# Kernel optimization log

Hardware: AMD Instinct MI355X
Metric: run time of the kernel (lower is better)

The kernel has to match this reference:

```python
import jax, jax.numpy as jnp
import numpy as np

# Model dims (match init_kwargs)
HID = 1024   # hidden_size
H   = 16     # num_heads
DK  = 64     # head_dim (key)
DV  = 128    # head value dim = int(head_dim * expand_v)
VAL = H * DV # value_dim = 2048
CONV = 4     # short conv kernel size
EPS = 1e-6
NORM_EPS = 1e-5


def _causal_conv_silu(x, w):
    # x: [B,T,C], w: [C,K] depthwise causal conv, no bias, silu activation
    T = x.shape[1]
    K = w.shape[1]
    xp = jnp.pad(x, ((0, 0), (K - 1, 0), (0, 0)))
    y = sum(xp[:, i:i + T, :] * w[:, i] for i in range(K))
    return jax.nn.silu(y)


def setup_inputs() -> dict:
    key = jax.random.key(0)
    ks = jax.random.split(key, 16)
    s = 0.02
    rn = lambda k, sh: jax.random.normal(k, sh, jnp.float32)
    return {
        'hidden_states': rn(ks[0], (1, 2048, HID)),
        'norm_w': jnp.ones((HID,), jnp.float32),
        'q_w': rn(ks[1], (H * DK, HID)) * s,
        'k_w': rn(ks[2], (H * DK, HID)) * s,
        'v_w': rn(ks[3], (VAL, HID)) * s,
        'a_w': rn(ks[4], (H, HID)) * s,
        'b_w': rn(ks[5], (H, HID)) * s,
        'g_w': rn(ks[6], (VAL, HID)) * s,
        'dt_bias': jax.random.uniform(ks[7], (H,), jnp.float32, -2.0, 0.0),
        'A_log': jnp.log(jax.random.uniform(ks[8], (H,), jnp.float32, 1.0, 8.0)),
        'conv_q_w': rn(ks[9], (H * DK, CONV)) * 0.2,
        'conv_k_w': rn(ks[10], (H * DK, CONV)) * 0.2,
        'conv_v_w': rn(ks[11], (VAL, CONV)) * 0.2,
        'o_norm_w': jnp.ones((DV,), jnp.float32),
        'o_proj_w': rn(ks[12], (HID, VAL)) * s,
        'out_proj_w': rn(ks[13], (HID, HID)) * s,
    }


def reference(hidden_states, norm_w, q_w, k_w, v_w, a_w, b_w, g_w, dt_bias,
              A_log, conv_q_w, conv_k_w, conv_v_w, o_norm_w, o_proj_w, out_proj_w):
    B, T, D = hidden_states.shape
    # RMSNorm
    x = hidden_states * jax.lax.rsqrt(
        jnp.mean(hidden_states * hidden_states, -1, keepdims=True) + EPS) * norm_w

    # projections + causal depthwise short conv + silu
    q = _causal_conv_silu(x @ q_w.T, conv_q_w).reshape(B, T, H, DK)
    k = _causal_conv_silu(x @ k_w.T, conv_k_w).reshape(B, T, H, DK)
    v = _causal_conv_silu(x @ v_w.T, conv_v_w).reshape(B, T, H, DV)

    beta = jax.nn.sigmoid(x @ b_w.T)                       # [B,T,H]
    g = -jnp.exp(A_log) * jax.nn.softplus(x @ a_w.T + dt_bias)  # [B,T,H] log-decay

    # rank-1 DC removal on keys: (I - 1 1^T / DK) k, i.e. subtract per-head mean
    k = k - jnp.mean(k, -1, keepdims=True)

    # L2 normalize q, k along head dim; scale q
    q = q * jax.lax.rsqrt(jnp.sum(q * q, -1, keepdims=True) + EPS)
    k = k * jax.lax.rsqrt(jnp.sum(k * k, -1, keepdims=True) + EPS)
    q = q * (DK ** -0.5)

    # gated delta-rule recurrence over time (time-major scan)
    qT = q.transpose(1, 0, 2, 3)
    kT = k.transpose(1, 0, 2, 3)
    vT = v.transpose(1, 0, 2, 3)
    bT = beta.transpose(1, 0, 2)
    gT = g.transpose(1, 0, 2)

    def step(S, inp):
        qt, kt, vt, bt, gt = inp              # S: [B,H,DK,DV]
        S = S * jnp.exp(gt)[..., None, None]
        v_new = (vt - jnp.einsum('bhk,bhkv->bhv', kt, S)) * bt[..., None]
        S = S + jnp.einsum('bhk,bhv->bhkv', kt, v_new)
        o = jnp.einsum('bhk,bhkv->bhv', qt, S)
        return S, o

    S0 = jnp.zeros((B, H, DK, DV), x.dtype)
    _, oT = jax.lax.scan(step, S0, (qT, kT, vT, bT, gT))
    o = oT.transpose(1, 0, 2, 3)                           # [B,T,H,DV]

    # gated RMSNorm on output heads
    gate = (x @ g_w.T).reshape(B, T, H, DV)
    o = o * jax.lax.rsqrt(jnp.mean(o * o, -1, keepdims=True) + NORM_EPS) * o_norm_w
    o = o * jax.nn.silu(gate)

    o = o.reshape(B, T, VAL) @ o_proj_w.T                  # [B,T,HID]
    return o @ out_proj_w.T
```

## Files before the change

kernel.cpp:

```cpp
#include <hip/hip_runtime.h>
#include <math.h>

#define S72 72

typedef __bf16 bf16;
typedef __bf16 bf16x8 __attribute__((ext_vector_type(8)));
typedef __bf16 bf16x4v __attribute__((ext_vector_type(4)));
typedef __bf16 bf16x2v __attribute__((ext_vector_type(2)));
typedef float f32x4 __attribute__((ext_vector_type(4)));

__device__ __forceinline__ float wredsum(float v) {
#pragma unroll
  for (int off = 32; off > 0; off >>= 1) v += __shfl_xor(v, off, 64);
  return v;
}
__device__ __forceinline__ float sigmoidf_(float x) { return 1.f / (1.f + __expf(-x)); }

__device__ __forceinline__ int sxy(int row, int col) {
  return (row << 6) + ((((col >> 3) ^ (row & 7)) << 3) | (col & 7));
}
__device__ __forceinline__ int sx8(int row, int chunk) {
  return (row << 6) + ((chunk ^ (row & 7)) << 3);
}

__global__ __launch_bounds__(256) void k_pre(const float* __restrict__ h,
    const float* __restrict__ nw, const float* __restrict__ aw,
    const float* __restrict__ bw, const float* __restrict__ dtb,
    const float* __restrict__ alog, bf16* __restrict__ xb,
    float* __restrict__ graw, float* __restrict__ btb,
    const float* __restrict__ qw, const float* __restrict__ kw,
    const float* __restrict__ vw, const float* __restrict__ gw,
    const float* __restrict__ opw, const float* __restrict__ ow,
    bf16* qwb, bf16* kwb, bf16* vwb, bf16* gwb, bf16* opwb, bf16* owb) {
  __shared__ float red[4];
  __shared__ __align__(16) float xs[1024];
  int tid = threadIdx.x;
  if (blockIdx.x >= 2048) {
    long cb = blockIdx.x - 2048;
    for (long u = cb*256 + tid; u < 2359296; u += 4608l*256) {
      const float* src; bf16* dst; long l;
      if      (u <  262144) { src=qw;  dst=qwb;  l=u; }
      else if (u <  524288) { src=kw;  dst=kwb;  l=u-262144; }
      else if (u < 1048576) { src=vw;  dst=vwb;  l=u-524288; }
      else if (u < 1572864) { src=gw;  dst=gwb;  l=u-1048576; }
      else if (u < 2097152) { src=opw; dst=opwb; l=u-1572864; }
      else                  { src=ow;  dst=owb;  l=u-2097152; }
      float4 s = *(const float4*)(src + l*4);
      bf16x4v b; b[0]=(bf16)s.x; b[1]=(bf16)s.y; b[2]=(bf16)s.z; b[3]=(bf16)s.w;
      *(bf16x4v*)(dst + l*4) = b;
    }
    return;
  }
  int t = blockIdx.x;
  float4 hv = *(const float4*)(h + (size_t)t*1024 + tid*4);
  float ss = hv.x*hv.x + hv.y*hv.y + hv.z*hv.z + hv.w*hv.w;
  float wsum = wredsum(ss);
  if ((tid & 63) == 0) red[tid >> 6] = wsum;
  __syncthreads();
  float tot = red[0] + red[1] + red[2] + red[3];
  float rs = rsqrtf(tot * (1.f/1024.f) + 1e-6f);
  float4 w4 = *(const float4*)(nw + tid*4);
  float4 y;
  y.x = hv.x*rs*w4.x; y.y = hv.y*rs*w4.y; y.z = hv.z*rs*w4.z; y.w = hv.w*rs*w4.w;
  *(float4*)(xs + tid*4) = y;
  bf16x4v b; b[0]=(bf16)y.x; b[1]=(bf16)y.y; b[2]=(bf16)y.z; b[3]=(bf16)y.w;
  *(bf16x4v*)(xb + (size_t)t*1024 + tid*4) = b;
  __syncthreads();
  int wave = tid >> 6, lane = tid & 63;
  const float4* x4 = (const float4*)xs;
#pragma unroll
  for (int hi = 0; hi < 4; ++hi) {
    int hh = wave*4 + hi;
    float sa = 0.f, sb = 0.f;
#pragma unroll
    for (int i = 0; i < 4; ++i) {
      float4 xv = x4[i*64 + lane];
      float4 av = *(const float4*)(aw + hh*1024 + i*256 + lane*4);
      float4 bv = *(const float4*)(bw + hh*1024 + i*256 + lane*4);
      sa += xv.x*av.x + xv.y*av.y + xv.z*av.z + xv.w*av.w;
      sb += xv.x*bv.x + xv.y*bv.y + xv.z*bv.z + xv.w*bv.w;
    }
    sa = wredsum(sa); sb = wredsum(sb);
    if (lane == 0) {
      float ap = sa + dtb[hh];
      float sp = (ap > 20.f) ? ap : log1pf(expf(ap));
      graw[t*16 + hh] = -expf(alog[hh]) * sp;
      btb[t*16 + hh] = 1.f / (1.f + expf(-sb));
    }
  }
}

template <typename OutT>
__device__ __forceinline__ void gemm_body(const bf16* __restrict__ A,
    const bf16* __restrict__ B, OutT* __restrict__ C, int N, int K, int m0, int n0) {
  __shared__ bf16 As[2][128*32];
  __shared__ bf16 Bs[2][128*32];
  const int tid = threadIdx.x, lane = tid & 63, wave = tid >> 6;
  const int wm = (wave >> 1) * 64, wn = (wave & 1) * 64;
  const int srow = wave*16 + (lane >> 2);
  const int swl = (((lane & 3) ^ ((lane >> 3) & 3))) * 8;
  const int sdst = (lane & 3) * 8;
  const int quad = lane >> 4, l16 = lane & 15;
  const int sw = (l16 >> 1) & 3;
  f32x4 acc[4][4] = {};
  const int nk = K >> 5;
#pragma unroll
  for (int i = 0; i < 2; ++i) {
    int r = i*64 + srow;
    __builtin_amdgcn_global_load_lds(
      (__attribute__((address_space(1))) void*)(A + (size_t)(m0 + r)*K + swl),
      (__attribute__((address_space(3))) void*)(&As[0][r*32 + sdst]), 16, 0, 0);
    __builtin_amdgcn_global_load_lds(
      (__attribute__((address_space(1))) void*)(B + (size_t)(n0 + r)*K + swl),
      (__attribute__((address_space(3))) void*)(&Bs[0][r*32 + sdst]), 16, 0, 0);
  }
  for (int kt = 0; kt < nk; ++kt) {
    const int cur = kt & 1;
    __syncthreads();
    bf16x8 af[4], bfr[4];
#pragma unroll
    for (int mt = 0; mt < 4; ++mt)
      af[mt] = *(const bf16x8*)(&As[cur][(wm + mt*16 + l16)*32 + (quad ^ sw)*8]);
#pragma unroll
    for (int nt = 0; nt < 4; ++nt)
      bfr[nt] = *(const bf16x8*)(&Bs[cur][(wn + nt*16 + l16)*32 + (quad ^ sw)*8]);
    if (kt + 1 < nk) {
      int k0 = (kt + 1) << 5;
#pragma unroll
      for (int i = 0; i < 2; ++i) {
        int r = i*64 + srow;
        __builtin_amdgcn_global_load_lds(
          (__attribute__((address_space(1))) void*)(A + (size_t)(m0 + r)*K + k0 + swl),
          (__attribute__((address_space(3))) void*)(&As[cur^1][r*32 + sdst]), 16, 0, 0);
        __builtin_amdgcn_global_load_lds(
          (__attribute__((address_space(1))) void*)(B + (size_t)(n0 + r)*K + k0 + swl),
          (__attribute__((address_space(3))) void*)(&Bs[cur^1][r*32 + sdst]), 16, 0, 0);
      }
    }
#pragma unroll
    for (int mt = 0; mt < 4; ++mt)
#pragma unroll
      for (int nt = 0; nt < 4; ++nt)
        acc[mt][nt] = __builtin_amdgcn_mfma_f32_16x16x32_bf16(af[mt], bfr[nt], acc[mt][nt], 0, 0, 0);
  }
#pragma unroll
  for (int mt = 0; mt < 4; ++mt)
#pragma unroll
    for (int nt = 0; nt < 4; ++nt)
#pragma unroll
      for (int r = 0; r < 4; ++r) {
        int row = m0 + wm + mt*16 + quad*4 + r;
        int col = n0 + wn + nt*16 + l16;
        C[(size_t)row*N + col] = (OutT)acc[mt][nt][r];
      }
}

__global__ __launch_bounds__(256) void k_gemm_proj(const bf16* __restrict__ A,
    const bf16* __restrict__ qwb, const bf16* __restrict__ kwb,
    const bf16* __restrict__ vwb, const bf16* __restrict__ gwb,
    bf16* __restrict__ qpre, bf16* __restrict__ kpre,
    bf16* __restrict__ vpre, bf16* __restrict__ gpre) {
  int bx = blockIdx.x;
  const bf16* B; bf16* C; int N, xt;
  if      (bx <  8) { B = qwb; C = qpre; N = 1024; xt = bx; }
  else if (bx < 16) { B = kwb; C = kpre; N = 1024; xt = bx - 8; }
  else if (bx < 32) { B = vwb; C = vpre; N = 2048; xt = bx - 16; }
  else              { B = gwb; C = gpre; N = 2048; xt = bx - 32; }
  gemm_body<bf16>(A, B, C, N, 1024, blockIdx.y*128, xt*128);
}

template <typename OutT>
__global__ __launch_bounds__(256) void k_gemm_bt64(const bf16* __restrict__ A,
    const bf16* __restrict__ B, OutT* __restrict__ C, int N, int K) {
  __shared__ bf16 As[2][128*32];
  __shared__ bf16 Bs[2][64*32];
  const int tid = threadIdx.x, lane = tid & 63, wave = tid >> 6;
  const int wm = wave * 32;
  const int srow = wave*16 + (lane >> 2);
  const int swl = (((lane & 3) ^ ((lane >> 3) & 3))) * 8;
  const int sdst = (lane & 3) * 8;
  const int quad = lane >> 4, l16 = lane & 15;
  const int sw = (l16 >> 1) & 3;
  const int m0 = blockIdx.y * 128, n0 = blockIdx.x * 64;
  f32x4 acc[2][4] = {};
  const int nk = K >> 5;
#pragma unroll
  for (int i = 0; i < 2; ++i) {
    int r = i*64 + srow;
    __builtin_amdgcn_global_load_lds(
      (__attribute__((address_space(1))) void*)(A + (size_t)(m0 + r)*K + swl),
      (__attribute__((address_space(3))) void*)(&As[0][r*32 + sdst]), 16, 0, 0);
  }
  __builtin_amdgcn_global_load_lds(
    (__attribute__((address_space(1))) void*)(B + (size_t)(n0 + srow)*K + swl),
    (__attribute__((address_space(3))) void*)(&Bs[0][srow*32 + sdst]), 16, 0, 0);
  for (int kt = 0; kt < nk; ++kt) {
    const int cur = kt & 1;
    __syncthreads();
    bf16x8 af[2], bfr[4];
#pragma unroll
    for (int mt = 0; mt < 2; ++mt)
      af[mt] = *(const bf16x8*)(&As[cur][(wm + mt*16 + l16)*32 + (quad ^ sw)*8]);
#pragma unroll
    for (int nt = 0; nt < 4; ++nt)
      bfr[nt] = *(const bf16x8*)(&Bs[cur][(nt*16 + l16)*32 + (quad ^ sw)*8]);
    if (kt + 1 < nk) {
      int k0 = (kt + 1) << 5;
#pragma unroll
      for (int i = 0; i < 2; ++i) {
        int r = i*64 + srow;
        __builtin_amdgcn_global_load_lds(
          (__attribute__((address_space(1))) void*)(A + (size_t)(m0 + r)*K + k0 + swl),
          (__attribute__((address_space(3))) void*)(&As[cur^1][r*32 + sdst]), 16, 0, 0);
      }
      __builtin_amdgcn_global_load_lds(
        (__attribute__((address_space(1))) void*)(B + (size_t)(n0 + srow)*K + k0 + swl),
        (__attribute__((address_space(3))) void*)(&Bs[cur^1][srow*32 + sdst]), 16, 0, 0);
    }
#pragma unroll
    for (int mt = 0; mt < 2; ++mt)
#pragma unroll
      for (int nt = 0; nt < 4; ++nt)
        acc[mt][nt] = __builtin_amdgcn_mfma_f32_16x16x32_bf16(af[mt], bfr[nt], acc[mt][nt], 0, 0, 0);
  }
#pragma unroll
  for (int mt = 0; mt < 2; ++mt)
#pragma unroll
    for (int nt = 0; nt < 4; ++nt)
#pragma unroll
      for (int r = 0; r < 4; ++r) {
        int row = m0 + wm + mt*16 + quad*4 + r;
        int col = n0 + nt*16 + l16;
        C[(size_t)row*N + col] = (OutT)acc[mt][nt][r];
      }
}

template<int NT>
__device__ __forceinline__ void mm_band(const bf16* A_lds, const bf16* B_lds,
    int w16, int cb, int l16, int quad, f32x4* acc) {
#pragma unroll
  for (int n = 0; n < NT; ++n) { acc[n][0]=0.f; acc[n][1]=0.f; acc[n][2]=0.f; acc[n][3]=0.f; }
#pragma unroll
  for (int kt = 0; kt < 2; ++kt) {
    bf16x8 af = *(const bf16x8*)(A_lds + sx8(w16 + l16, kt*4 + quad));
#pragma unroll
    for (int n = 0; n < NT; ++n) {
      bf16x8 bf = *(const bf16x8*)(B_lds + sx8(cb + n*16 + l16, kt*4 + quad));
      acc[n] = __builtin_amdgcn_mfma_f32_16x16x32_bf16(af, bf, acc[n], 0, 0, 0);
    }
  }
}

__global__ __launch_bounds__(512) void k_prepass(
    const bf16* __restrict__ qpre, const bf16* __restrict__ kpre,
    const bf16* __restrict__ vpre, const float* __restrict__ cqw,
    const float* __restrict__ ckw, const float* __restrict__ cvw,
    const float* __restrict__ graw, const float* __restrict__ beta,
    bf16* __restrict__ EF, float* __restrict__ dSl, float* __restrict__ obuf) {
  const int bx = blockIdx.x, c = bx >> 4, h = bx & 15, tid = threadIdx.x;
  const int t0 = c * 64;
  const int wave = tid >> 6, lane = tid & 63, l16 = lane & 15, quad = lane >> 4;
  const int w16 = (wave >> 1) * 16;
  const int chh = wave & 1;
  const int r0 = wave * 8;

  __shared__ bf16 SM[36864];
  __shared__ float bs[64], bts_s[64], es[64], gms[64];
  bf16* Kr    = SM;
  bf16* powR0 = SM + 4096;
  bf16* prod0 = SM + 8192;
  bf16* T2T   = SM + 12288;
  bf16* powT0 = SM + 16384;
  bf16* powR1 = SM + 20480;
  bf16* powT1 = SM + 24576;
  bf16* prod1 = SM + 28672;
  bf16* qbf   = SM + 32768;
  bf16* VT   = SM;
  bf16* VlT  = SM + 8192;
  bf16* KT   = powT0;
  bf16* KbT  = powR1;
  bf16* Pm   = powT1;
  bf16* WR   = prod0;
  bf16* Mrow = prod1;

  if (tid < 64) {
    float g = graw[(size_t)(t0 + tid)*16 + h];
    float b = g;
#pragma unroll
    for (int off = 1; off < 64; off <<= 1) {
      float p = __shfl_up(b, off, 64);
      if (tid >= off) b += p;
    }
    bs[tid] = b;
    bts_s[tid] = beta[(size_t)(t0 + tid)*16 + h];
    float b63 = __shfl(b, 63, 64);
    es[tid] = __expf(b63 - b);
    gms[tid] = __expf(b);
  }

  float kreg[8], vreg[16];
  {
    float4 wq  = *(const float4*)(cqw + (h*64 + lane)*4);
    float4 wk  = *(const float4*)(ckw + (h*64 + lane)*4);
    float tv[11];
#pragma unroll
    for (int j = 0; j < 11; ++j) {
      int tg = t0 + r0 + j - 3;
      tv[j] = (tg >= 0) ? (float)qpre[(size_t)tg*1024 + h*64 + lane] : 0.f;
    }
#pragma unroll
    for (int rr = 0; rr < 8; ++rr) {
      float y = tv[rr]*wq.x + tv[rr+1]*wq.y + tv[rr+2]*wq.z + tv[rr+3]*wq.w;
      y = y * sigmoidf_(y);
      float ssq = wredsum(y*y);
      y *= rsqrtf(ssq + 1e-6f) * 0.125f;
      qbf[sxy(r0+rr, lane)] = (bf16)y;
    }
#pragma unroll
    for (int j = 0; j < 11; ++j) {
      int tg = t0 + r0 + j - 3;
      tv[j] = (tg >= 0) ? (float)kpre[(size_t)tg*1024 + h*64 + lane] : 0.f;
    }
#pragma unroll
    for (int rr = 0; rr < 8; ++rr) {
      float y = tv[rr]*wk.x + tv[rr+1]*wk.y + tv[rr+2]*wk.z + tv[rr+3]*wk.w;
      y = y * sigmoidf_(y);
      float m = wredsum(y) * (1.f/64.f);
      y -= m;
      float ssq = wredsum(y*y);
      y *= rsqrtf(ssq + 1e-6f);
      kreg[rr] = y;
      Kr[sxy(r0+rr, lane)] = (bf16)y;
    }
#pragma unroll
    for (int hf = 0; hf < 2; ++hf) {
      float4 wv = *(const float4*)(cvw + (h*128 + hf*64 + lane)*4);
#pragma unroll
      for (int j = 0; j < 11; ++j) {
        int tg = t0 + r0 + j - 3;
        tv[j] = (tg >= 0) ? (float)vpre[(size_t)tg*2048 + h*128 + hf*64 + lane] : 0.f;
      }
#pragma unroll
      for (int rr = 0; rr < 8; ++rr) {
        float y = tv[rr]*wv.x + tv[rr+1]*wv.y + tv[rr+2]*wv.z + tv[rr+3]*wv.w;
        vreg[hf*8+rr] = y * sigmoidf_(y);
      }
    }
  }
  __syncthreads();

  {
    f32x4 acc[2];
    mm_band<2>(Kr, Kr, w16, chh*32, l16, quad, acc);
#pragma unroll
    for (int n = 0; n < 2; ++n) {
      int col = chh*32 + n*16 + l16;
      bf16x4v tv;
#pragma unroll
      for (int r = 0; r < 4; ++r) {
        int row = w16 + quad*4 + r;
        float nv = 0.f;
        if (row > col) nv = -bts_s[row] * __expf(bs[row] - bs[col]) * acc[n][r];
        bf16 nb = (bf16)nv;
        powR0[sxy(row, col)] = nb;
        tv[r] = nb;
        prod0[sxy(row, col)] = (row == col) ? (bf16)1.f : nb;
      }
      *(bf16x4v*)(powT0 + sxy(col, w16 + quad*4)) = tv;
    }
  }
  __syncthreads();

  int pc = 0, rc = 0;
#pragma unroll 1
  for (int i = 1; i <= 5; ++i) {
    bf16* sqA = pc ? powR1 : powR0;
    bf16* sqB = pc ? powT1 : powT0;
    bf16* sqRo = pc ? powR0 : powR1;
    bf16* sqTo = pc ? powT0 : powT1;
    {
      f32x4 acc[2];
      mm_band<2>(sqA, sqB, w16, chh*32, l16, quad, acc);
#pragma unroll
      for (int n = 0; n < 2; ++n) {
        int col = chh*32 + n*16 + l16;
        bf16x4v tv;
#pragma unroll
        for (int r = 0; r < 4; ++r) {
          int row = w16 + quad*4 + r;
          bf16 vb = (bf16)acc[n][r];
          sqRo[sxy(row, col)] = vb;
          tv[r] = vb;
        }
        *(bf16x4v*)(sqTo + sxy(col, w16 + quad*4)) = tv;
      }
    }
    __syncthreads();
    bf16* prA = rc ? prod1 : prod0;
    bf16* prO = rc ? prod0 : prod1;
    {
      f32x4 acc[2];
      mm_band<2>(prA, sqTo, w16, chh*32, l16, quad, acc);
#pragma unroll
      for (int n = 0; n < 2; ++n) {
        int col = chh*32 + n*16 + l16;
        bf16x4v tv;
#pragma unroll
        for (int r = 0; r < 4; ++r) {
          int row = w16 + quad*4 + r;
          float val = acc[n][r] + (float)prA[sxy(row, col)];
          prO[sxy(row, col)] = (bf16)val;
          tv[r] = (bf16)(val * bts_s[col] * gms[col]);
        }
        if (i == 5) *(bf16x4v*)(T2T + sxy(col, w16 + quad*4)) = tv;
      }
    }
    __syncthreads();
    pc ^= 1; rc ^= 1;
  }

#pragma unroll
  for (int rr = 0; rr < 8; ++rr) {
    KT[sxy(lane, r0+rr)]  = (bf16)kreg[rr];
    KbT[sxy(lane, r0+rr)] = (bf16)(kreg[rr] * es[r0+rr]);
  }
  {
    f32x4 acc[2];
#pragma unroll
    for (int n = 0; n < 2; ++n) { acc[n][0]=0.f; acc[n][1]=0.f; acc[n][2]=0.f; acc[n][3]=0.f; }
#pragma unroll
    for (int kt = 0; kt < 2; ++kt) {
      bf16x8 af = *(const bf16x8*)(qbf + sx8(w16 + l16, kt*4 + quad));
#pragma unroll
      for (int n = 0; n < 2; ++n) {
        bf16x8 bf = *(const bf16x8*)(Kr + sx8(chh*32 + n*16 + l16, kt*4 + quad));
        acc[n] = __builtin_amdgcn_mfma_f32_16x16x32_bf16(af, bf, acc[n], 0, 0, 0);
      }
    }
#pragma unroll
    for (int n = 0; n < 2; ++n) {
      int col = chh*32 + n*16 + l16;
#pragma unroll
      for (int r = 0; r < 4; ++r) {
        int row = w16 + quad*4 + r;
        float pv = (row >= col) ? __expf(bs[row] - bs[col]) * acc[n][r] : 0.f;
        Pm[sxy(row, col)] = (bf16)pv;
      }
    }
  }
  __syncthreads();

  {
    f32x4 acc[2];
    mm_band<2>(KbT, T2T, w16, chh*32, l16, quad, acc);
#pragma unroll
    for (int n = 0; n < 2; ++n) {
      int col = chh*32 + n*16 + l16;
#pragma unroll
      for (int r = 0; r < 4; ++r)
        WR[sxy(w16 + quad*4 + r, col)] = (bf16)acc[n][r];
    }
  }
#pragma unroll
  for (int hf = 0; hf < 2; ++hf)
#pragma unroll
    for (int rr = 0; rr < 8; ++rr)
      VT[sxy(hf*64 + lane, r0+rr)] = (bf16)(bts_s[r0+rr] * vreg[hf*8+rr]);
  __syncthreads();
  {
    f32x4 acc[2];
    mm_band<2>(WR, KT, w16, chh*32, l16, quad, acc);
    float gC = gms[63];
    size_t eb = (size_t)bx * 13824;
#pragma unroll
    for (int n = 0; n < 2; ++n) {
      int col = chh*32 + n*16 + l16;
#pragma unroll
      for (int r = 0; r < 4; ++r) {
        int row = w16 + quad*4 + r;
        float ev = ((row == col) ? gC : 0.f) - acc[n][r];
        bf16 eh = (bf16)ev;
        EF[eb + row*S72 + col] = eh;
        EF[eb + 4608 + row*S72 + col] = (bf16)(ev - (float)eh);
      }
    }
  }
  __syncthreads();
  {
    f32x4 acc[2];
    mm_band<2>(Pm, T2T, w16, chh*32, l16, quad, acc);
#pragma unroll
    for (int n = 0; n < 2; ++n) {
      int col = chh*32 + n*16 + l16;
#pragma unroll
      for (int r = 0; r < 4; ++r)
        WR[sxy(w16 + quad*4 + r, col)] = (bf16)acc[n][r];
    }
  }
  __syncthreads();
  {
    f32x4 acc[2];
    mm_band<2>(WR, KT, w16, chh*32, l16, quad, acc);
    size_t eb = (size_t)bx * 13824;
#pragma unroll
    for (int n = 0; n < 2; ++n) {
      int col = chh*32 + n*16 + l16;
#pragma unroll
      for (int r = 0; r < 4; ++r) {
        int row = w16 + quad*4 + r;
        float qv = (float)qbf[sxy(row, col)];
        EF[eb + 9216 + row*S72 + col] = (bf16)(gms[row]*qv - acc[n][r]);
      }
    }
  }
  __syncthreads();
  {
    f32x4 acc[4];
    mm_band<4>(Mrow, VT, w16, chh*64, l16, quad, acc);
#pragma unroll
    for (int n = 0; n < 4; ++n) {
      int col = chh*64 + n*16 + l16;
      bf16x4v tv;
#pragma unroll
      for (int r = 0; r < 4; ++r) tv[r] = (bf16)acc[n][r];
      *(bf16x4v*)(VlT + sxy(col, w16 + quad*4)) = tv;
    }
  }
  __syncthreads();
  {
    f32x4 acc[4];
    mm_band<4>(KbT, VlT, w16, chh*64, l16, quad, acc);
#pragma unroll
    for (int n = 0; n < 4; ++n) {
      int col = chh*64 + n*16 + l16;
#pragma unroll
      for (int r = 0; r < 4; ++r)
        dSl[(size_t)bx*8192 + (size_t)(w16 + quad*4 + r)*128 + col] = acc[n][r];
    }
  }
  {
    f32x4 acc[4];
    mm_band<4>(Pm, VlT, w16, chh*64, l16, quad, acc);
#pragma unroll
    for (int n = 0; n < 4; ++n) {
      int col = chh*64 + n*16 + l16;
#pragma unroll
      for (int r = 0; r < 4; ++r)
        obuf[(size_t)(t0 + w16 + quad*4 + r)*2048 + h*128 + col] = acc[n][r];
    }
  }
}

__global__ __launch_bounds__(256) void k_seq(const bf16* __restrict__ EF,
    const float* __restrict__ dSl, float* __restrict__ osb) {
  const int bid = blockIdx.x;
  const int h = (bid & 7) + 8*((bid >> 3) & 1);
  const int dq = bid >> 4;
  const int tid = threadIdx.x, wave = tid >> 6, lane = tid & 63;
  const int l16 = lane & 15, quad = lane >> 4;
  const int mb = wave * 16;
  __shared__ bf16 Sthi[32*S72], Stlo[32*S72];
  for (int i = tid; i < 2304; i += 256) { Sthi[i] = (bf16)0.f; Stlo[i] = (bf16)0.f; }

  const size_t arow = (size_t)(mb + l16)*S72 + quad*8;
  const size_t drow = (size_t)dq*32 + (size_t)(mb + quad*4)*128 + l16;

  bf16x8 eh[2][2], el[2][2], ff[2][2];
  float dsv[2][8];

  auto loadEF = [&](int c, int sl) {
    const bf16* base = EF + (size_t)(c*16 + h)*13824 + arow;
#pragma unroll
    for (int kt = 0; kt < 2; ++kt) {
      eh[sl][kt] = *(const bf16x8*)(base + kt*32);
      el[sl][kt] = *(const bf16x8*)(base + 4608 + kt*32);
      ff[sl][kt] = *(const bf16x8*)(base + 9216 + kt*32);
    }
    const float* db = dSl + (size_t)(c*16 + h)*8192 + drow;
#pragma unroll
    for (int nt = 0; nt < 2; ++nt)
#pragma unroll
      for (int r = 0; r < 4; ++r)
        dsv[sl][nt*4+r] = db[(size_t)r*128 + nt*16];
  };

  loadEF(0, 0);
  asm volatile("s_waitcnt lgkmcnt(0)" ::: "memory");
  __builtin_amdgcn_s_barrier();

#pragma unroll 2
  for (int c = 0; c < 32; ++c) {
    const int cur = c & 1, nxt = cur ^ 1;
    bf16x8 bh[2][2], bl[2][2];
#pragma unroll
    for (int nt = 0; nt < 2; ++nt)
#pragma unroll
      for (int kt = 0; kt < 2; ++kt) {
        bh[nt][kt] = *(const bf16x8*)(Sthi + (nt*16 + l16)*S72 + kt*32 + quad*8);
        bl[nt][kt] = *(const bf16x8*)(Stlo + (nt*16 + l16)*S72 + kt*32 + quad*8);
      }
    if (c + 1 < 32) loadEF(c + 1, nxt);

    f32x4 accS[2], accO[2];
#pragma unroll
    for (int nt = 0; nt < 2; ++nt) {
#pragma unroll
      for (int r = 0; r < 4; ++r) accS[nt][r] = dsv[cur][nt*4+r];
      accO[nt][0]=0.f; accO[nt][1]=0.f; accO[nt][2]=0.f; accO[nt][3]=0.f;
    }
#pragma unroll
    for (int kt = 0; kt < 2; ++kt) {
#pragma unroll
      for (int nt = 0; nt < 2; ++nt) {
        accS[nt] = __builtin_amdgcn_mfma_f32_16x16x32_bf16(eh[cur][kt], bh[nt][kt], accS[nt], 0, 0, 0);
        accS[nt] = __builtin_amdgcn_mfma_f32_16x16x32_bf16(eh[cur][kt], bl[nt][kt], accS[nt], 0, 0, 0);
        accS[nt] = __builtin_amdgcn_mfma_f32_16x16x32_bf16(el[cur][kt], bh[nt][kt], accS[nt], 0, 0, 0);
        accO[nt] = __builtin_amdgcn_mfma_f32_16x16x32_bf16(ff[cur][kt], bh[nt][kt], accO[nt], 0, 0, 0);
        accO[nt] = __builtin_amdgcn_mfma_f32_16x16x32_bf16(ff[cur][kt], bl[nt][kt], accO[nt], 0, 0, 0);
      }
    }
    asm volatile("s_waitcnt lgkmcnt(0)" ::: "memory");
    __builtin_amdgcn_s_barrier();
    {
      int t0 = c*64;
#pragma unroll
      for (int nt = 0; nt < 2; ++nt)
#pragma unroll
        for (int r = 0; r < 4; ++r)
          osb[(size_t)(t0 + mb + quad*4 + r)*2048 + h*128 + dq*32 + nt*16 + l16] = accO[nt][r];
    }
#pragma unroll
    for (int nt = 0; nt < 2; ++nt) {
      bf16x4v hv, lv;
#pragma unroll
      for (int r = 0; r < 4; ++r) {
        float v = accS[nt][r];
        bf16 hb = (bf16)v;
        hv[r] = hb;
        lv[r] = (bf16)(v - (float)hb);
      }
      *(bf16x4v*)(Sthi + (nt*16 + l16)*S72 + mb + quad*4) = hv;
      *(bf16x4v*)(Stlo + (nt*16 + l16)*S72 + mb + quad*4) = lv;
    }
    asm volatile("s_waitcnt lgkmcnt(0)" ::: "memory");
    __builtin_amdgcn_s_barrier();
  }
}

__global__ __launch_bounds__(64) void k_gatenorm(const float* __restrict__ o,
    const float* __restrict__ os, const bf16* __restrict__ gpre,
    const float* __restrict__ onw, bf16* __restrict__ og) {
  int t = blockIdx.x, hh = blockIdx.y, lane = threadIdx.x;
  size_t base = (size_t)t*2048 + hh*128 + lane*2;
  float2 o2 = *(const float2*)(o + base);
  float2 s2 = *(const float2*)(os + base);
  o2.x += s2.x; o2.y += s2.y;
  float ss = wredsum(o2.x*o2.x + o2.y*o2.y);
  float rs = rsqrtf(ss * (1.f/128.f) + 1e-5f);
  float2 nw = *(const float2*)(onw + lane*2);
  bf16x2v g2 = *(const bf16x2v*)(gpre + base);
  float g0 = (float)g2[0], g1 = (float)g2[1];
  float r0 = o2.x * rs * nw.x * (g0 * sigmoidf_(g0));
  float r1 = o2.y * rs * nw.y * (g1 * sigmoidf_(g1));
  bf16x2v b; b[0] = (bf16)r0; b[1] = (bf16)r1;
  *(bf16x2v*)(og + base) = b;
}

extern "C" void kernel_launch(void* const* d_in, const int* in_sizes, int n_in,
                              void* d_out, int out_size, void* d_ws, size_t ws_size,
                              hipStream_t stream) {
  const float* hs   = (const float*)d_in[0];
  const float* nw   = (const float*)d_in[1];
  const float* qw   = (const float*)d_in[2];
  const float* kw   = (const float*)d_in[3];
  const float* vw   = (const float*)d_in[4];
  const float* aw   = (const float*)d_in[5];
  const float* bw   = (const float*)d_in[6];
  const float* gw   = (const float*)d_in[7];
  const float* dtb  = (const float*)d_in[8];
  const float* alog = (const float*)d_in[9];
  const float* cqw  = (const float*)d_in[10];
  const float* ckw  = (const float*)d_in[11];
  const float* cvw  = (const float*)d_in[12];
  const float* onw  = (const float*)d_in[13];
  const float* opw  = (const float*)d_in[14];
  const float* ow   = (const float*)d_in[15];
  float* out = (float*)d_out;

  char* p = (char*)d_ws;
  auto alloc = [&](size_t bytes) { char* r = p; p += (bytes + 255) & ~255ull; return r; };
  bf16*  xb    = (bf16*) alloc((size_t)2048*1024*2);
  bf16*  qwb   = (bf16*) alloc((size_t)1024*1024*2);
  bf16*  kwb   = (bf16*) alloc((size_t)1024*1024*2);
  bf16*  vwb   = (bf16*) alloc((size_t)2048*1024*2);
  bf16*  gwb   = (bf16*) alloc((size_t)2048*1024*2);
  bf16*  opwb  = (bf16*) alloc((size_t)1024*2048*2);
  bf16*  owb   = (bf16*) alloc((size_t)1024*1024*2);
  bf16*  qpre  = (bf16*) alloc((size_t)2048*1024*2);
  bf16*  kpre  = (bf16*) alloc((size_t)2048*1024*2);
  bf16*  vpre  = (bf16*) alloc((size_t)2048*2048*2);
  bf16*  gpre  = (bf16*) alloc((size_t)2048*2048*2);
  float* graw  = (float*)alloc((size_t)2048*16*4);
  float* btb   = (float*)alloc((size_t)2048*16*4);
  float* ob    = (float*)alloc((size_t)2048*2048*4);
  bf16*  ogb   = (bf16*) alloc((size_t)2048*2048*2);
  bf16*  h1b   = (bf16*) alloc((size_t)2048*1024*2);
  bf16*  EF    = (bf16*) alloc((size_t)512*13824*2);
  float* osb   = (float*)alloc((size_t)512*8192*4);
  float* dSl   = (float*)xb;

  k_pre<<<2048+4608, 256, 0, stream>>>(hs, nw, aw, bw, dtb, alog, xb, graw, btb,
                                       qw, kw, vw, gw, opw, ow,
                                       qwb, kwb, vwb, gwb, opwb, owb);
  k_gemm_proj<<<dim3(48,16,1), 256, 0, stream>>>(xb, qwb, kwb, vwb, gwb, qpre, kpre, vpre, gpre);
  k_prepass<<<512, 512, 0, stream>>>(qpre, kpre, vpre, cqw, ckw, cvw, graw, btb, EF, dSl, ob);
  k_seq<<<64, 256, 0, stream>>>(EF, dSl, osb);
  k_gatenorm<<<dim3(2048,16,1), 64, 0, stream>>>(ob, osb, gpre, onw, ogb);
  k_gemm_bt64<bf16><<<dim3(16,16,1), 256, 0, stream>>>(ogb, opwb, h1b, 1024, 2048);
  k_gemm_bt64<float><<<dim3(16,16,1), 256, 0, stream>>>(h1b, owb, out, 1024, 1024);
}
```

Before: 272.0 us.

## Double-buffer state in sequential scan, split MFMA chains, batch conv loads in prepass

The sequential chunk kernel now keeps the bf16 hi/lo state in two LDS buffers, ping-ponging between them. This removes one of the two barriers per chunk, and the five MFMA products use independent accumulators so the dependent MFMA chains are shorter. In the prepass, the q/k/v conv input loads are issued together up front, and the k mean and variance reductions run in one fused shuffle loop; launch bounds now carry an occupancy hint. The changes add LDS use and register pressure, and the one-pass variance formula is slightly less numerically robust.

```diff
diff --git a/kernel.cpp b/kernel.cpp
--- a/kernel.cpp
+++ b/kernel.cpp
@@ -251,7 +251,7 @@
   }
 }
 
-__global__ __launch_bounds__(512) void k_prepass(
+__global__ __launch_bounds__(512, 4) void k_prepass(
     const bf16* __restrict__ qpre, const bf16* __restrict__ kpre,
     const bf16* __restrict__ vpre, const float* __restrict__ cqw,
     const float* __restrict__ ckw, const float* __restrict__ cvw,
@@ -302,49 +302,49 @@
   {
     float4 wq  = *(const float4*)(cqw + (h*64 + lane)*4);
     float4 wk  = *(const float4*)(ckw + (h*64 + lane)*4);
-    float tv[11];
+    float4 wv0 = *(const float4*)(cvw + (h*128 + lane)*4);
+    float4 wv1 = *(const float4*)(cvw + (h*128 + 64 + lane)*4);
+    float qtv[11], ktv[11], vtv0[11], vtv1[11];
 #pragma unroll
     for (int j = 0; j < 11; ++j) {
       int tg = t0 + r0 + j - 3;
-      tv[j] = (tg >= 0) ? (float)qpre[(size_t)tg*1024 + h*64 + lane] : 0.f;
+      bool ok = tg >= 0;
+      qtv[j]  = ok ? (float)qpre[(size_t)tg*1024 + h*64 + lane] : 0.f;
+      ktv[j]  = ok ? (float)kpre[(size_t)tg*1024 + h*64 + lane] : 0.f;
+      vtv0[j] = ok ? (float)vpre[(size_t)tg*2048 + h*128 + lane] : 0.f;
+      vtv1[j] = ok ? (float)vpre[(size_t)tg*2048 + h*128 + 64 + lane] : 0.f;
     }
 #pragma unroll
     for (int rr = 0; rr < 8; ++rr) {
-      float y = tv[rr]*wq.x + tv[rr+1]*wq.y + tv[rr+2]*wq.z + tv[rr+3]*wq.w;
+      float y = qtv[rr]*wq.x + qtv[rr+1]*wq.y + qtv[rr+2]*wq.z + qtv[rr+3]*wq.w;
       y = y * sigmoidf_(y);
       float ssq = wredsum(y*y);
       y *= rsqrtf(ssq + 1e-6f) * 0.125f;
       qbf[sxy(r0+rr, lane)] = (bf16)y;
     }
 #pragma unroll
-    for (int j = 0; j < 11; ++j) {
-      int tg = t0 + r0 + j - 3;
-      tv[j] = (tg >= 0) ? (float)kpre[(size_t)tg*1024 + h*64 + lane] : 0.f;
-    }
-#pragma unroll
     for (int rr = 0; rr < 8; ++rr) {
-      float y = tv[rr]*wk.x + tv[rr+1]*wk.y + tv[rr+2]*wk.z + tv[rr+3]*wk.w;
+      float y = ktv[rr]*wk.x + ktv[rr+1]*wk.y + ktv[rr+2]*wk.z + ktv[rr+3]*wk.w;
       y = y * sigmoidf_(y);
-      float m = wredsum(y) * (1.f/64.f);
+      float s1 = y, s2 = y*y;
+#pragma unroll
+      for (int off = 32; off > 0; off >>= 1) {
+        s1 += __shfl_xor(s1, off, 64);
+        s2 += __shfl_xor(s2, off, 64);
+      }
+      float m = s1 * (1.f/64.f);
+      float ssq = s2 - s1*m;
       y -= m;
-      float ssq = wredsum(y*y);
       y *= rsqrtf(ssq + 1e-6f);
       kreg[rr] = y;
       Kr[sxy(r0+rr, lane)] = (bf16)y;
     }
 #pragma unroll
-    for (int hf = 0; hf < 2; ++hf) {
-      float4 wv = *(const float4*)(cvw + (h*128 + hf*64 + lane)*4);
-#pragma unroll
-      for (int j = 0; j < 11; ++j) {
-        int tg = t0 + r0 + j - 3;
-        tv[j] = (tg >= 0) ? (float)vpre[(size_t)tg*2048 + h*128 + hf*64 + lane] : 0.f;
-      }
-#pragma unroll
-      for (int rr = 0; rr < 8; ++rr) {
-        float y = tv[rr]*wv.x + tv[rr+1]*wv.y + tv[rr+2]*wv.z + tv[rr+3]*wv.w;
-        vreg[hf*8+rr] = y * sigmoidf_(y);
-      }
+    for (int rr = 0; rr < 8; ++rr) {
+      float y0 = vtv0[rr]*wv0.x + vtv0[rr+1]*wv0.y + vtv0[rr+2]*wv0.z + vtv0[rr+3]*wv0.w;
+      float y1 = vtv1[rr]*wv1.x + vtv1[rr+1]*wv1.y + vtv1[rr+2]*wv1.z + vtv1[rr+3]*wv1.w;
+      vreg[rr]   = y0 * sigmoidf_(y0);
+      vreg[8+rr] = y1 * sigmoidf_(y1);
     }
   }
   __syncthreads();
@@ -559,8 +559,8 @@
   const int tid = threadIdx.x, wave = tid >> 6, lane = tid & 63;
   const int l16 = lane & 15, quad = lane >> 4;
   const int mb = wave * 16;
-  __shared__ bf16 Sthi[32*S72], Stlo[32*S72];
-  for (int i = tid; i < 2304; i += 256) { Sthi[i] = (bf16)0.f; Stlo[i] = (bf16)0.f; }
+  __shared__ bf16 Sthi[2][32*S72], Stlo[2][32*S72];
+  for (int i = tid; i < 2304; i += 256) { Sthi[0][i] = (bf16)0.f; Stlo[0][i] = (bf16)0.f; }
 
   const size_t arow = (size_t)(mb + l16)*S72 + quad*8;
   const size_t drow = (size_t)dq*32 + (size_t)(mb + quad*4)*128 + l16;
@@ -596,51 +596,50 @@
     for (int nt = 0; nt < 2; ++nt)
 #pragma unroll
       for (int kt = 0; kt < 2; ++kt) {
-        bh[nt][kt] = *(const bf16x8*)(Sthi + (nt*16 + l16)*S72 + kt*32 + quad*8);
-        bl[nt][kt] = *(const bf16x8*)(Stlo + (nt*16 + l16)*S72 + kt*32 + quad*8);
+        bh[nt][kt] = *(const bf16x8*)(&Sthi[cur][(nt*16 + l16)*S72 + kt*32 + quad*8]);
+        bl[nt][kt] = *(const bf16x8*)(&Stlo[cur][(nt*16 + l16)*S72 + kt*32 + quad*8]);
       }
     if (c + 1 < 32) loadEF(c + 1, nxt);
 
-    f32x4 accS[2], accO[2];
-#pragma unroll
-    for (int nt = 0; nt < 2; ++nt) {
-#pragma unroll
-      for (int r = 0; r < 4; ++r) accS[nt][r] = dsv[cur][nt*4+r];
-      accO[nt][0]=0.f; accO[nt][1]=0.f; accO[nt][2]=0.f; accO[nt][3]=0.f;
-    }
-#pragma unroll
-    for (int kt = 0; kt < 2; ++kt) {
+    f32x4 a1[2], a2[2], a3[2], o1[2], o2[2];
+#pragma unroll
+    for (int nt = 0; nt < 2; ++nt)
+#pragma unroll
+      for (int r = 0; r < 4; ++r) {
+        a1[nt][r] = dsv[cur][nt*4+r];
+        a2[nt][r] = 0.f; a3[nt][r] = 0.f; o1[nt][r] = 0.f; o2[nt][r] = 0.f;
+      }
+#pragma unroll
+    for (int kt = 0; kt < 2; ++kt)
 #pragma unroll
       for (int nt = 0; nt < 2; ++nt) {
-        accS[nt] = __builtin_amdgcn_mfma_f32_16x16x32_bf16(eh[cur][kt], bh[nt][kt], accS[nt], 0, 0, 0);
-        accS[nt] = __builtin_amdgcn_mfma_f32_16x16x32_bf16(eh[cur][kt], bl[nt][kt], accS[nt], 0, 0, 0);
-        accS[nt] = __builtin_amdgcn_mfma_f32_16x16x32_bf16(el[cur][kt], bh[nt][kt], accS[nt], 0, 0, 0);
-        accO[nt] = __builtin_amdgcn_mfma_f32_16x16x32_bf16(ff[cur][kt], bh[nt][kt], accO[nt], 0, 0, 0);
-        accO[nt] = __builtin_amdgcn_mfma_f32_16x16x32_bf16(ff[cur][kt], bl[nt][kt], accO[nt], 0, 0, 0);
-      }
-    }
-    asm volatile("s_waitcnt lgkmcnt(0)" ::: "memory");
-    __builtin_amdgcn_s_barrier();
+        a1[nt] = __builtin_amdgcn_mfma_f32_16x16x32_bf16(eh[cur][kt], bh[nt][kt], a1[nt], 0, 0, 0);
+        a2[nt] = __builtin_amdgcn_mfma_f32_16x16x32_bf16(eh[cur][kt], bl[nt][kt], a2[nt], 0, 0, 0);
+        a3[nt] = __builtin_amdgcn_mfma_f32_16x16x32_bf16(el[cur][kt], bh[nt][kt], a3[nt], 0, 0, 0);
+        o1[nt] = __builtin_amdgcn_mfma_f32_16x16x32_bf16(ff[cur][kt], bh[nt][kt], o1[nt], 0, 0, 0);
+        o2[nt] = __builtin_amdgcn_mfma_f32_16x16x32_bf16(ff[cur][kt], bl[nt][kt], o2[nt], 0, 0, 0);
+      }
     {
-      int t0 = c*64;
+      int t0c = c*64;
 #pragma unroll
       for (int nt = 0; nt < 2; ++nt)
 #pragma unroll
         for (int r = 0; r < 4; ++r)
-          osb[(size_t)(t0 + mb + quad*4 + r)*2048 + h*128 + dq*32 + nt*16 + l16] = accO[nt][r];
+          osb[(size_t)(t0c + mb + quad*4 + r)*2048 + h*128 + dq*32 + nt*16 + l16]
+            = o1[nt][r] + o2[nt][r];
     }
 #pragma unroll
     for (int nt = 0; nt < 2; ++nt) {
       bf16x4v hv, lv;
 #pragma unroll
       for (int r = 0; r < 4; ++r) {
-        float v = accS[nt][r];
+        float v = a1[nt][r] + a2[nt][r] + a3[nt][r];
         bf16 hb = (bf16)v;
         hv[r] = hb;
         lv[r] = (bf16)(v - (float)hb);
       }
-      *(bf16x4v*)(Sthi + (nt*16 + l16)*S72 + mb + quad*4) = hv;
-      *(bf16x4v*)(Stlo + (nt*16 + l16)*S72 + mb + quad*4) = lv;
+      *(bf16x4v*)(&Sthi[nxt][(nt*16 + l16)*S72 + mb + quad*4]) = hv;
+      *(bf16x4v*)(&Stlo[nxt][(nt*16 + l16)*S72 + mb + quad*4]) = lv;
     }
     asm volatile("s_waitcnt lgkmcnt(0)" ::: "memory");
     __builtin_amdgcn_s_barrier();
```

Result: faster. 266.1 us (-2.2%).
